# Optimization experiments

Measured on AMD Instinct MI355X. Metric: run time of the kernel, lower is better.

## Reference

```python
import jax, jax.numpy as jnp
import numpy as np

B, T, DIM, H, BUCKET = 4, 4096, 1024, 16, 64
E = DIM // H          # head dim = 64
U = T // BUCKET       # number of buckets = 64
EPS = 1e-6


def setup_inputs() -> dict:
    key = jax.random.key(0)
    ks = jax.random.split(key, 5)
    scale = 1.0 / np.sqrt(DIM)
    return {
        "x": jax.random.normal(ks[0], (B, T, DIM), dtype=jnp.float32),
        "Wq": jax.random.normal(ks[1], (DIM, DIM), dtype=jnp.float32) * scale,
        "Wk": jax.random.normal(ks[2], (DIM, DIM), dtype=jnp.float32) * scale,
        "Wv": jax.random.normal(ks[3], (DIM, DIM), dtype=jnp.float32) * scale,
        "Wo": jax.random.normal(ks[4], (DIM, DIM), dtype=jnp.float32) * scale,
        "bo": jnp.zeros((DIM,), dtype=jnp.float32),
    }


def _causal_linear_attn(q, k, v):
    # q, k, v: [b, h, t, e]; psi(k) = elu(k) + 1; q softmaxed over feature dim
    q = jax.nn.softmax(q, axis=-1)
    k = jax.nn.elu(k) + 1.0
    bucket = lambda x: x.reshape(*x.shape[:-2], U, BUCKET, E)  # [b,h,u,n,e]
    b_q, b_k, b_v = bucket(q), bucket(k), bucket(v)
    # cumulative key sums per bucket: [b,h,u,d]
    b_k_cumsum = jnp.cumsum(b_k.sum(axis=-2), axis=2)
    # per-bucket context then cumulative over buckets: [b,h,u,d,e]
    context = jnp.einsum("bhund,bhune->bhude", b_k, b_v)
    context = jnp.cumsum(context, axis=2)
    context = context / (b_k_cumsum[..., None] + EPS)
    # shift by one bucket (blindspot): bucket u sees context through bucket u-1
    context = jnp.concatenate(
        [jnp.zeros_like(context[:, :, :1]), context[:, :, :-1]], axis=2
    )
    attn = jnp.einsum("bhund,bhude->bhune", b_q, context)
    return attn.reshape(q.shape)  # [b,h,t,e]


def reference(x, Wq, Wk, Wv, Wo, bo):
    b, t, _ = x.shape
    q = x @ Wq
    k = x @ Wk
    v = x @ Wv
    merge = lambda z: z.reshape(b, t, H, E).transpose(0, 2, 1, 3)  # [b,h,t,e]
    attn = _causal_linear_attn(merge(q), merge(k), merge(v))
    out = attn.transpose(0, 2, 1, 3).reshape(b, t, DIM)
    return out @ Wo + bo
```

## Files before the change

### kernel.cpp

```cpp
#include <hip/hip_runtime.h>


#define T_LEN 4096
#define DIMN  1024
#define NHEAD 16
#define NB    4
#define MROWS (NB * T_LEN)

typedef float f32x4 __attribute__((ext_vector_type(4)));
typedef short s16x8 __attribute__((ext_vector_type(8)));
typedef short s16x4 __attribute__((ext_vector_type(4)));
using u16 = unsigned short;

__device__ __forceinline__ u16 f2bf(float f) {
  unsigned int u = __float_as_uint(f);
  u += 0x7fffu + ((u >> 16) & 1u);
  return (u16)(u >> 16);
}
__device__ __forceinline__ float bf2f(u16 h) {
  return __uint_as_float(((unsigned int)h) << 16);
}
__device__ __forceinline__ int swz16k(int off) {
  return off ^ (((off >> 7) & 3) << 4);
}

__global__ __launch_bounds__(256) void cvt_w_kern(const float* __restrict__ W0,
                                                  const float* __restrict__ W1,
                                                  const float* __restrict__ W2,
                                                  const float* __restrict__ W3,
                                                  u16* __restrict__ WT) {
  __shared__ float tile[64][65];
  const int blk = blockIdx.x & 255;
  const int sel = blockIdx.x >> 8;
  const float* W = (sel == 0) ? W0 : (sel == 1) ? W1 : (sel == 2) ? W2 : W3;
  u16* dst = WT + (size_t)sel * DIMN * DIMN;
  const int k0 = (blk >> 4) << 6;
  const int n0 = (blk & 15) << 6;
  const int tid = threadIdx.x;
  const int r = tid >> 6;
  const int c = tid & 63;
#pragma unroll
  for (int i = 0; i < 16; ++i) {
    int row = (i << 2) + r;
    tile[row][c] = W[(size_t)(k0 + row) * DIMN + n0 + c];
  }
  __syncthreads();
#pragma unroll
  for (int i = 0; i < 16; ++i) {
    int row = (i << 2) + r;
    dst[(size_t)(n0 + row) * DIMN + k0 + c] = f2bf(tile[c][row]);
  }
}

__global__ __launch_bounds__(256) void cvt_x_kern(const float* __restrict__ x,
                                                  u16* __restrict__ xb) {
  size_t i = ((size_t)blockIdx.x * 256 + threadIdx.x) * 4;
  f32x4 v = *(const f32x4*)(x + i);
  s16x4 o;
  o.x = (short)f2bf(v.x); o.y = (short)f2bf(v.y);
  o.z = (short)f2bf(v.z); o.w = (short)f2bf(v.w);
  *(s16x4*)(xb + i) = o;
}

template <int MODE>
__global__ __launch_bounds__(512, 2) void gemm256(
    const u16* __restrict__ A, const u16* __restrict__ Bt,
    u16* __restrict__ dq, u16* __restrict__ dk, u16* __restrict__ dv,
    float* __restrict__ dO, const float* __restrict__ bias) {
  constexpr int K = 1024;
  constexpr int BNT = (MODE == 0) ? 12 : 4;
  constexpr int NT = K / 64;
  extern __shared__ char lds[];

  const int tid = threadIdx.x;
  const int l = tid & 63;
  const int w = tid >> 6;
  const int wm = w >> 2;
  const int wn = w & 3;

  const int nwg = (int)gridDim.x;
  const int bid = (int)blockIdx.x;
  const int swz = (bid & 7) * (nwg >> 3) + (bid >> 3);
  const int bm = swz / BNT, bn = swz % BNT;
  const size_t arow0 = (size_t)bm * 256;
  const size_t brow0 = (size_t)bn * 256;

  int lrow[2], lcol[2];
#pragma unroll
  for (int i = 0; i < 2; ++i) {
    int lg = swz16k(tid * 16 + i * 8192);
    lrow[i] = lg >> 6;
    lcol[i] = (lg & 63) >> 1;
  }

  const int fr = l & 15;
  const int kswz = (((l >> 4) << 4)) ^ ((((fr >> 1) & 3)) << 4);

  auto STAGE = [&](int matsel, int kh, int tt) {
    const int kbase = (tt & (NT - 1)) * 64 + kh * 32;
#pragma unroll
    for (int i = 0; i < 2; ++i) {
      const u16* src = (matsel == 0)
          ? A  + (arow0 + (size_t)lrow[i]) * K + kbase + lcol[i]
          : Bt + (brow0 + (size_t)lrow[i]) * K + kbase + lcol[i];
      char* dst = lds + ((tt & 1) * 65536 + (matsel * 2 + kh) * 16384 +
                         i * 8192 + w * 1024);
      __builtin_amdgcn_global_load_lds(
          (__attribute__((address_space(1))) const void*)src,
          (__attribute__((address_space(3))) void*)dst, 16, 0, 0);
    }
  };
  auto LDA = [&](int buf, int kh, int rowb) -> s16x8 {
    return *(const s16x8*)(lds + buf * 65536 + kh * 16384 + rowb * 64 + kswz);
  };
  auto LDB = [&](int buf, int kh, int rowb) -> s16x8 {
    return *(const s16x8*)(lds + buf * 65536 + 32768 + kh * 16384 + rowb * 64 + kswz);
  };

  f32x4 acc[8][4];
#pragma unroll
  for (int i = 0; i < 8; ++i)
#pragma unroll
    for (int j = 0; j < 4; ++j) acc[i][j] = {0.f, 0.f, 0.f, 0.f};

  STAGE(0, 0, 0); STAGE(1, 0, 0); STAGE(0, 1, 0); STAGE(1, 1, 0);
  STAGE(0, 0, 1); STAGE(1, 0, 1);
  asm volatile("s_waitcnt vmcnt(8)" ::: "memory");
  __builtin_amdgcn_sched_barrier(0);
  __builtin_amdgcn_s_barrier();

  const int amb = wm * 128;
  const int bnb = wn * 64;
  s16x8 af[4], bfr[4];

  for (int t = 0; t < NT; ++t) {
    const int buf = t & 1;
    __builtin_amdgcn_sched_barrier(0);
#pragma unroll
    for (int i = 0; i < 4; ++i) af[i]  = LDA(buf, 0, amb + i * 16 + fr);
#pragma unroll
    for (int i = 0; i < 4; ++i) bfr[i] = LDB(buf, 0, bnb + i * 16 + fr);
    STAGE(0, 1, t + 1);
    __builtin_amdgcn_s_setprio(1);
#pragma unroll
    for (int mi = 0; mi < 4; ++mi)
#pragma unroll
      for (int ni = 0; ni < 4; ++ni)
        acc[mi][ni] = __builtin_amdgcn_mfma_f32_16x16x32_bf16(
            af[mi], bfr[ni], acc[mi][ni], 0, 0, 0);
    __builtin_amdgcn_s_setprio(0);
    __builtin_amdgcn_s_barrier();
    __builtin_amdgcn_sched_barrier(0);
#pragma unroll
    for (int i = 0; i < 4; ++i) af[i] = LDA(buf, 0, amb + (4 + i) * 16 + fr);
    STAGE(1, 1, t + 1);
    __builtin_amdgcn_s_setprio(1);
#pragma unroll
    for (int mi = 0; mi < 4; ++mi)
#pragma unroll
      for (int ni = 0; ni < 4; ++ni)
        acc[4 + mi][ni] = __builtin_amdgcn_mfma_f32_16x16x32_bf16(
            af[mi], bfr[ni], acc[4 + mi][ni], 0, 0, 0);
    __builtin_amdgcn_s_setprio(0);
    asm volatile("s_waitcnt vmcnt(8)" ::: "memory");
    __builtin_amdgcn_sched_barrier(0);
    __builtin_amdgcn_s_barrier();
    __builtin_amdgcn_sched_barrier(0);
#pragma unroll
    for (int i = 0; i < 4; ++i) af[i]  = LDA(buf, 1, amb + i * 16 + fr);
#pragma unroll
    for (int i = 0; i < 4; ++i) bfr[i] = LDB(buf, 1, bnb + i * 16 + fr);
    STAGE(0, 0, t + 2);
    __builtin_amdgcn_s_setprio(1);
#pragma unroll
    for (int mi = 0; mi < 4; ++mi)
#pragma unroll
      for (int ni = 0; ni < 4; ++ni)
        acc[mi][ni] = __builtin_amdgcn_mfma_f32_16x16x32_bf16(
            af[mi], bfr[ni], acc[mi][ni], 0, 0, 0);
    __builtin_amdgcn_s_setprio(0);
    __builtin_amdgcn_s_barrier();
    __builtin_amdgcn_sched_barrier(0);
#pragma unroll
    for (int i = 0; i < 4; ++i) af[i] = LDA(buf, 1, amb + (4 + i) * 16 + fr);
    STAGE(1, 0, t + 2);
    __builtin_amdgcn_s_setprio(1);
#pragma unroll
    for (int mi = 0; mi < 4; ++mi)
#pragma unroll
      for (int ni = 0; ni < 4; ++ni)
        acc[4 + mi][ni] = __builtin_amdgcn_mfma_f32_16x16x32_bf16(
            af[mi], bfr[ni], acc[4 + mi][ni], 0, 0, 0);
    __builtin_amdgcn_s_setprio(0);
    asm volatile("s_waitcnt vmcnt(8)" ::: "memory");
    __builtin_amdgcn_sched_barrier(0);
    __builtin_amdgcn_s_barrier();
  }

  asm volatile("s_waitcnt vmcnt(0)" ::: "memory");
  __builtin_amdgcn_sched_barrier(0);
  __builtin_amdgcn_s_barrier();

  const int r0 = (l >> 4) << 2;
  const int c0 = l & 15;
  if constexpr (MODE == 0) {
    u16* lt = (u16*)lds;
    const int mat = bn >> 2;
    u16* dst = (mat == 0) ? dq : ((mat == 1) ? dk : dv);
    if (mat == 0) {
#pragma unroll
      for (int mi = 0; mi < 8; ++mi) {
#pragma unroll
        for (int j = 0; j < 4; ++j) {
          float v0 = acc[mi][0][j], v1 = acc[mi][1][j];
          float v2 = acc[mi][2][j], v3 = acc[mi][3][j];
          float m = fmaxf(fmaxf(v0, v1), fmaxf(v2, v3));
#pragma unroll
          for (int off = 1; off < 16; off <<= 1) m = fmaxf(m, __shfl_xor(m, off));
          float e0 = __expf(v0 - m), e1 = __expf(v1 - m);
          float e2 = __expf(v2 - m), e3 = __expf(v3 - m);
          float s = e0 + e1 + e2 + e3;
#pragma unroll
          for (int off = 1; off < 16; off <<= 1) s += __shfl_xor(s, off);
          float inv = 1.f / s;
          const int row = wm * 128 + mi * 16 + r0 + j;
          const int sxr = ((row >> 2) & 7) << 4;
          const int cb = wn * 64 + c0;
          lt[row * 256 + ((cb) ^ sxr)]      = f2bf(e0 * inv);
          lt[row * 256 + ((cb + 16) ^ sxr)] = f2bf(e1 * inv);
          lt[row * 256 + ((cb + 32) ^ sxr)] = f2bf(e2 * inv);
          lt[row * 256 + ((cb + 48) ^ sxr)] = f2bf(e3 * inv);
        }
      }
    } else {
#pragma unroll
      for (int mi = 0; mi < 8; ++mi)
#pragma unroll
        for (int ni = 0; ni < 4; ++ni)
#pragma unroll
          for (int j = 0; j < 4; ++j) {
            const int row = wm * 128 + mi * 16 + r0 + j;
            const int col = wn * 64 + ni * 16 + c0;
            float v = acc[mi][ni][j];
            float r = (mat == 1) ? (v > 0.f ? v + 1.f : __expf(v)) : v;
            lt[row * 256 + (col ^ (((row >> 2) & 7) << 4))] = f2bf(r);
          }
    }
    __builtin_amdgcn_s_barrier();
    const size_t gcb = (size_t)(bn & 3) * 256;
#pragma unroll
    for (int i = 0; i < 16; ++i) {
      const int cid = tid + i * 512;
      const int r = cid >> 5;
      const int g = (cid & 31) * 8;
      const int pc = g ^ (((r >> 2) & 7) << 4);
      s16x8 vv = *(const s16x8*)&lt[r * 256 + pc];
      *(s16x8*)&dst[(arow0 + r) * DIMN + gcb + g] = vv;
    }
  } else {
    float* lf = (float*)lds;
#pragma unroll
    for (int half = 0; half < 2; ++half) {
      if (wm == half) {
#pragma unroll
        for (int mi = 0; mi < 8; ++mi)
#pragma unroll
          for (int ni = 0; ni < 4; ++ni) {
            const int col = wn * 64 + ni * 16 + c0;
            const float bv = bias[brow0 + col];
#pragma unroll
            for (int j = 0; j < 4; ++j) {
              const int row = mi * 16 + r0 + j;
              lf[row * 256 + (col ^ (((row >> 2) & 1) << 4))] =
                  acc[mi][ni][j] + bv;
            }
          }
      }
      __builtin_amdgcn_s_barrier();
#pragma unroll
      for (int i = 0; i < 16; ++i) {
        const int cid = tid + i * 512;
        const int r = cid >> 6;
        const int g = (cid & 63) * 4;
        const int pc = g ^ (((r >> 2) & 1) << 4);
        f32x4 vv = *(const f32x4*)&lf[r * 256 + pc];
        *(f32x4*)&dO[(arow0 + half * 128 + r) * DIMN + brow0 + g] = vv;
      }
      __builtin_amdgcn_s_barrier();
    }
  }
}

__global__ __launch_bounds__(256) void ctx_bucket_kern(const u16* __restrict__ kb,
                                                       const u16* __restrict__ vb,
                                                       float* __restrict__ ctx,
                                                       float* __restrict__ ksum) {
  __shared__ float kl[4096];
  __shared__ float vl[4096];
  const int blk = blockIdx.x;
  const int u = blk & 63;
  const int bh = blk >> 6;
  const int b = bh >> 4, h = bh & 15;
  const size_t rowbase = (size_t)b * T_LEN + (size_t)u * 64;
  const int tid = threadIdx.x;
#pragma unroll
  for (int i = 0; i < 16; ++i) {
    int idx = i * 256 + tid;
    int n = idx >> 6, d = idx & 63;
    size_t g = (rowbase + n) * DIMN + (size_t)h * 64 + d;
    kl[idx] = bf2f(kb[g]);
    vl[idx] = bf2f(vb[g]);
  }
  __syncthreads();
  const int dq = (tid & 15) << 2;
  const int eq = (tid >> 4) << 2;
  float a[4][4] = {};
  float ks[4] = {};
  for (int n = 0; n < 64; ++n) {
    f32x4 kv = *(const f32x4*)&kl[n * 64 + dq];
    f32x4 vv = *(const f32x4*)&vl[n * 64 + eq];
#pragma unroll
    for (int i = 0; i < 4; ++i) {
      ks[i] += kv[i];
#pragma unroll
      for (int j = 0; j < 4; ++j) a[i][j] += kv[i] * vv[j];
    }
  }
  const size_t cbase = (size_t)blk * 4096;
#pragma unroll
  for (int i = 0; i < 4; ++i) {
    f32x4 o = {a[i][0], a[i][1], a[i][2], a[i][3]};
    *(f32x4*)&ctx[cbase + (size_t)(dq + i) * 64 + eq] = o;
  }
  if ((tid >> 4) == 0) {
    f32x4 o = {ks[0], ks[1], ks[2], ks[3]};
    *(f32x4*)&ksum[(size_t)blk * 64 + dq] = o;
  }
}

__global__ __launch_bounds__(256) void ctx_cumnorm_kern(float* __restrict__ ctx,
                                                        const float* __restrict__ ksum) {
  const int tid = blockIdx.x * 256 + threadIdx.x;
  const int bh = tid >> 12;
  const int rem = tid & 4095;
  const int d = rem >> 6;
  const int e = rem & 63;
  float c = 0.f, accK = 0.f;
  for (int u = 0; u < 64; ++u) {
    const size_t base = ((size_t)(bh * 64 + u)) * 4096 + (size_t)d * 64 + e;
    float cv = ctx[base];
    float kk = ksum[(size_t)(bh * 64 + u) * 64 + d];
    float o = (u == 0) ? 0.f : c / (accK + 1e-6f);
    ctx[base] = o;
    c += cv; accK += kk;
  }
}

__global__ __launch_bounds__(256) void attn_bucket_kern(const u16* __restrict__ qb,
                                                        const float* __restrict__ ctx,
                                                        u16* __restrict__ attn) {
  __shared__ float qT[64 * 68];
  __shared__ float cl[4096];
  const int blk = blockIdx.x;
  const int u = blk & 63;
  const int bh = blk >> 6;
  const int b = bh >> 4, h = bh & 15;
  const size_t rowbase = (size_t)b * T_LEN + (size_t)u * 64;
  const int tid = threadIdx.x;
  const size_t cbase = (size_t)blk * 4096;
#pragma unroll
  for (int i = 0; i < 16; ++i) {
    int idx = i * 256 + tid;
    int n = idx >> 6, d = idx & 63;
    qT[d * 68 + n] = bf2f(qb[(rowbase + n) * DIMN + (size_t)h * 64 + d]);
    cl[idx] = ctx[cbase + idx];
  }
  __syncthreads();
  const int nq = (tid & 15) << 2;
  const int eq = (tid >> 4) << 2;
  float a[4][4] = {};
  for (int d = 0; d < 64; ++d) {
    f32x4 qv = *(const f32x4*)&qT[d * 68 + nq];
    f32x4 cv = *(const f32x4*)&cl[d * 64 + eq];
#pragma unroll
    for (int i = 0; i < 4; ++i)
#pragma unroll
      for (int j = 0; j < 4; ++j) a[i][j] += qv[i] * cv[j];
  }
#pragma unroll
  for (int i = 0; i < 4; ++i) {
    s16x4 o;
    o.x = (short)f2bf(a[i][0]); o.y = (short)f2bf(a[i][1]);
    o.z = (short)f2bf(a[i][2]); o.w = (short)f2bf(a[i][3]);
    *(s16x4*)&attn[(rowbase + nq + i) * DIMN + (size_t)h * 64 + eq] = o;
  }
}

extern "C" void kernel_launch(void* const* d_in, const int* in_sizes, int n_in,
                              void* d_out, int out_size, void* d_ws, size_t ws_size,
                              hipStream_t stream) {
  const float* x  = (const float*)d_in[0];
  const float* Wq = (const float*)d_in[1];
  const float* Wk = (const float*)d_in[2];
  const float* Wv = (const float*)d_in[3];
  const float* Wo = (const float*)d_in[4];
  const float* bo = (const float*)d_in[5];
  float* out = (float*)d_out;

  constexpr size_t SZ_XB = (size_t)MROWS * DIMN * 2;
  constexpr size_t SZ_WT = (size_t)DIMN * DIMN * 2;
  constexpr size_t SZ_CTX = (size_t)NB * NHEAD * 64 * 64 * 64 * 4;
  char* ws = (char*)d_ws;
  u16*   xb   = (u16*)(ws);
  u16*   wqT  = (u16*)(ws + SZ_XB);
  u16*   woT  = (u16*)(ws + SZ_XB + 3 * SZ_WT);
  u16*   qb   = (u16*)(ws + SZ_XB + 4 * SZ_WT);
  u16*   kb   = (u16*)(ws + 2 * SZ_XB + 4 * SZ_WT);
  u16*   vb   = (u16*)(ws + 3 * SZ_XB + 4 * SZ_WT);
  float* ctx  = (float*)(ws + 4 * SZ_XB + 4 * SZ_WT);
  float* ksum = (float*)(ws + 4 * SZ_XB + 4 * SZ_WT + SZ_CTX);
  u16*   attn = xb;

  (void)hipFuncSetAttribute((const void*)gemm256<0>,
                            hipFuncAttributeMaxDynamicSharedMemorySize, 131072);
  (void)hipFuncSetAttribute((const void*)gemm256<1>,
                            hipFuncAttributeMaxDynamicSharedMemorySize, 131072);

  cvt_w_kern<<<1024, 256, 0, stream>>>(Wq, Wk, Wv, Wo, wqT);
  cvt_x_kern<<<MROWS * DIMN / 4 / 256, 256, 0, stream>>>(x, xb);

  gemm256<0><<<768, 512, 131072, stream>>>(xb, wqT, qb, kb, vb, nullptr, nullptr);

  ctx_bucket_kern<<<NB * NHEAD * 64, 256, 0, stream>>>(kb, vb, ctx, ksum);
  ctx_cumnorm_kern<<<1024, 256, 0, stream>>>(ctx, ksum);
  attn_bucket_kern<<<NB * NHEAD * 64, 256, 0, stream>>>(qb, ctx, attn);

  gemm256<1><<<256, 512, 131072, stream>>>(attn, woT, nullptr, nullptr, nullptr, out, bo);
}
```

Before: 284.4 us.

## Double-buffer MFMA fragment registers and write QKV epilogue directly to global

The GEMM main loop now prefetches the next phase's LDS fragments into a second register set (afA/afB, bfA/bfB) while the current MFMA block runs. It unrolls two tiles per iteration with fewer sched barriers. For MODE 0 the epilogue drops the LDS staging and the coalesced copy-out, and each lane writes bf16 values straight to global memory. This removes a barrier and an LDS round trip, but the stores become scattered 2-byte writes, and register pressure rises from the extra fragment buffers.

```diff
diff --git a/kernel.cpp b/kernel.cpp
--- a/kernel.cpp
+++ b/kernel.cpp
@@ -131,82 +131,75 @@
 
   const int amb = wm * 128;
   const int bnb = wn * 64;
-  s16x8 af[4], bfr[4];
-
-  for (int t = 0; t < NT; ++t) {
-    const int buf = t & 1;
-    __builtin_amdgcn_sched_barrier(0);
-#pragma unroll
-    for (int i = 0; i < 4; ++i) af[i]  = LDA(buf, 0, amb + i * 16 + fr);
-#pragma unroll
-    for (int i = 0; i < 4; ++i) bfr[i] = LDB(buf, 0, bnb + i * 16 + fr);
-    STAGE(0, 1, t + 1);
-    __builtin_amdgcn_s_setprio(1);
-#pragma unroll
-    for (int mi = 0; mi < 4; ++mi)
-#pragma unroll
-      for (int ni = 0; ni < 4; ++ni)
-        acc[mi][ni] = __builtin_amdgcn_mfma_f32_16x16x32_bf16(
-            af[mi], bfr[ni], acc[mi][ni], 0, 0, 0);
-    __builtin_amdgcn_s_setprio(0);
-    __builtin_amdgcn_s_barrier();
-    __builtin_amdgcn_sched_barrier(0);
-#pragma unroll
-    for (int i = 0; i < 4; ++i) af[i] = LDA(buf, 0, amb + (4 + i) * 16 + fr);
-    STAGE(1, 1, t + 1);
-    __builtin_amdgcn_s_setprio(1);
-#pragma unroll
-    for (int mi = 0; mi < 4; ++mi)
-#pragma unroll
-      for (int ni = 0; ni < 4; ++ni)
-        acc[4 + mi][ni] = __builtin_amdgcn_mfma_f32_16x16x32_bf16(
-            af[mi], bfr[ni], acc[4 + mi][ni], 0, 0, 0);
-    __builtin_amdgcn_s_setprio(0);
-    asm volatile("s_waitcnt vmcnt(8)" ::: "memory");
-    __builtin_amdgcn_sched_barrier(0);
-    __builtin_amdgcn_s_barrier();
-    __builtin_amdgcn_sched_barrier(0);
-#pragma unroll
-    for (int i = 0; i < 4; ++i) af[i]  = LDA(buf, 1, amb + i * 16 + fr);
-#pragma unroll
-    for (int i = 0; i < 4; ++i) bfr[i] = LDB(buf, 1, bnb + i * 16 + fr);
-    STAGE(0, 0, t + 2);
-    __builtin_amdgcn_s_setprio(1);
-#pragma unroll
-    for (int mi = 0; mi < 4; ++mi)
-#pragma unroll
-      for (int ni = 0; ni < 4; ++ni)
-        acc[mi][ni] = __builtin_amdgcn_mfma_f32_16x16x32_bf16(
-            af[mi], bfr[ni], acc[mi][ni], 0, 0, 0);
-    __builtin_amdgcn_s_setprio(0);
-    __builtin_amdgcn_s_barrier();
-    __builtin_amdgcn_sched_barrier(0);
-#pragma unroll
-    for (int i = 0; i < 4; ++i) af[i] = LDA(buf, 1, amb + (4 + i) * 16 + fr);
-    STAGE(1, 0, t + 2);
-    __builtin_amdgcn_s_setprio(1);
-#pragma unroll
-    for (int mi = 0; mi < 4; ++mi)
-#pragma unroll
-      for (int ni = 0; ni < 4; ++ni)
-        acc[4 + mi][ni] = __builtin_amdgcn_mfma_f32_16x16x32_bf16(
-            af[mi], bfr[ni], acc[4 + mi][ni], 0, 0, 0);
-    __builtin_amdgcn_s_setprio(0);
-    asm volatile("s_waitcnt vmcnt(8)" ::: "memory");
-    __builtin_amdgcn_sched_barrier(0);
-    __builtin_amdgcn_s_barrier();
-  }
-
-  asm volatile("s_waitcnt vmcnt(0)" ::: "memory");
-  __builtin_amdgcn_sched_barrier(0);
-  __builtin_amdgcn_s_barrier();
+  s16x8 afA[4], afB[4], bfA[4], bfB[4];
+
+#pragma unroll
+  for (int i = 0; i < 4; ++i) afA[i] = LDA(0, 0, amb + i * 16 + fr);
+#pragma unroll
+  for (int i = 0; i < 4; ++i) bfA[i] = LDB(0, 0, bnb + i * 16 + fr);
+
+#define MFMA_BLK(ACCOFF, AF, BF)                                              \
+  __builtin_amdgcn_s_setprio(1);                                              \
+  _Pragma("unroll")                                                           \
+  for (int mi = 0; mi < 4; ++mi)                                              \
+    _Pragma("unroll")                                                         \
+    for (int ni = 0; ni < 4; ++ni)                                            \
+      acc[(ACCOFF) + mi][ni] = __builtin_amdgcn_mfma_f32_16x16x32_bf16(       \
+          AF[mi], BF[ni], acc[(ACCOFF) + mi][ni], 0, 0, 0);                   \
+  __builtin_amdgcn_s_setprio(0);
+
+#define PHASES(BUF, T)                                                        \
+  {                                                                           \
+    const int buf = (BUF);                                                    \
+    const int t = (T);                                                        \
+     \
+    STAGE(0, 1, t + 1);                                                       \
+    _Pragma("unroll")                                                         \
+    for (int i = 0; i < 4; ++i) afB[i] = LDA(buf, 0, amb + (4 + i) * 16 + fr);\
+    MFMA_BLK(0, afA, bfA)                                                     \
+    __builtin_amdgcn_s_barrier();                                             \
+      \
+    STAGE(1, 1, t + 1);                                                       \
+    asm volatile("s_waitcnt vmcnt(8)" ::: "memory");                          \
+    __builtin_amdgcn_sched_barrier(0);                                        \
+    _Pragma("unroll")                                                         \
+    for (int i = 0; i < 4; ++i) afA[i] = LDA(buf, 1, amb + i * 16 + fr);      \
+    _Pragma("unroll")                                                         \
+    for (int i = 0; i < 4; ++i) bfB[i] = LDB(buf, 1, bnb + i * 16 + fr);      \
+    MFMA_BLK(4, afB, bfA)                                                     \
+    __builtin_amdgcn_s_barrier();                                             \
+     \
+    STAGE(0, 0, t + 2);                                                       \
+    _Pragma("unroll")                                                         \
+    for (int i = 0; i < 4; ++i) afB[i] = LDA(buf, 1, amb + (4 + i) * 16 + fr);\
+    MFMA_BLK(0, afA, bfB)                                                     \
+    __builtin_amdgcn_s_barrier();                                             \
+       \
+    STAGE(1, 0, t + 2);                                                       \
+    asm volatile("s_waitcnt vmcnt(8)" ::: "memory");                          \
+    __builtin_amdgcn_sched_barrier(0);                                        \
+    _Pragma("unroll")                                                         \
+    for (int i = 0; i < 4; ++i) afA[i] = LDA(buf ^ 1, 0, amb + i * 16 + fr);  \
+    _Pragma("unroll")                                                         \
+    for (int i = 0; i < 4; ++i) bfA[i] = LDB(buf ^ 1, 0, bnb + i * 16 + fr);  \
+    MFMA_BLK(4, afB, bfB)                                                     \
+    __builtin_amdgcn_s_barrier();                                             \
+  }
+
+#pragma unroll 1
+  for (int th = 0; th < NT / 2; ++th) {
+    PHASES(0, 2 * th)
+    PHASES(1, 2 * th + 1)
+  }
+#undef PHASES
+#undef MFMA_BLK
 
   const int r0 = (l >> 4) << 2;
   const int c0 = l & 15;
   if constexpr (MODE == 0) {
-    u16* lt = (u16*)lds;
     const int mat = bn >> 2;
     u16* dst = (mat == 0) ? dq : ((mat == 1) ? dk : dv);
+    const size_t colbase = (size_t)(bn & 3) * 256 + (size_t)wn * 64;
     if (mat == 0) {
 #pragma unroll
       for (int mi = 0; mi < 8; ++mi) {
@@ -223,13 +216,10 @@
 #pragma unroll
           for (int off = 1; off < 16; off <<= 1) s += __shfl_xor(s, off);
           float inv = 1.f / s;
-          const int row = wm * 128 + mi * 16 + r0 + j;
-          const int sxr = ((row >> 2) & 7) << 4;
-          const int cb = wn * 64 + c0;
-          lt[row * 256 + ((cb) ^ sxr)]      = f2bf(e0 * inv);
-          lt[row * 256 + ((cb + 16) ^ sxr)] = f2bf(e1 * inv);
-          lt[row * 256 + ((cb + 32) ^ sxr)] = f2bf(e2 * inv);
-          lt[row * 256 + ((cb + 48) ^ sxr)] = f2bf(e3 * inv);
+          const size_t row = arow0 + wm * 128 + mi * 16 + r0 + j;
+          u16* p = dst + row * DIMN + colbase + c0;
+          p[0]  = f2bf(e0 * inv); p[16] = f2bf(e1 * inv);
+          p[32] = f2bf(e2 * inv); p[48] = f2bf(e3 * inv);
         }
       }
     } else {
@@ -239,25 +229,16 @@
         for (int ni = 0; ni < 4; ++ni)
 #pragma unroll
           for (int j = 0; j < 4; ++j) {
-            const int row = wm * 128 + mi * 16 + r0 + j;
-            const int col = wn * 64 + ni * 16 + c0;
+            const size_t row = arow0 + wm * 128 + mi * 16 + r0 + j;
             float v = acc[mi][ni][j];
             float r = (mat == 1) ? (v > 0.f ? v + 1.f : __expf(v)) : v;
-            lt[row * 256 + (col ^ (((row >> 2) & 7) << 4))] = f2bf(r);
+            dst[row * DIMN + colbase + ni * 16 + c0] = f2bf(r);
           }
     }
+  } else {
+    asm volatile("s_waitcnt vmcnt(0)" ::: "memory");
+    __builtin_amdgcn_sched_barrier(0);
     __builtin_amdgcn_s_barrier();
-    const size_t gcb = (size_t)(bn & 3) * 256;
-#pragma unroll
-    for (int i = 0; i < 16; ++i) {
-      const int cid = tid + i * 512;
-      const int r = cid >> 5;
-      const int g = (cid & 31) * 8;
-      const int pc = g ^ (((r >> 2) & 7) << 4);
-      s16x8 vv = *(const s16x8*)&lt[r * 256 + pc];
-      *(s16x8*)&dst[(arow0 + r) * DIMN + gcb + g] = vv;
-    }
-  } else {
     float* lf = (float*)lds;
 #pragma unroll
     for (int half = 0; half < 2; ++half) {
```

New measurement: 280.5 us. No clear change (-1.4%).
